# Kernel optimization log

Hardware: AMD Instinct MI355X
Metric: run time of the kernel (lower is better)

## Reference

```python
import jax, jax.numpy as jnp
import numpy as np
import math

# Model hyperparameters (SchNet defaults)
H = 128        # hidden_channels
F = 128        # num_filters
G = 50         # num_gaussians
CUT = 6.0      # cutoff (Angstrom)
L_INT = 3      # num_interactions
# Graph scale
N_MOL = 512    # molecules
APM = 32       # atoms per molecule
N = N_MOL * APM
BOX = 10.0     # side of cubic box per molecule


def _ssp(x):
    # ShiftedSoftplus
    return jax.nn.softplus(x) - math.log(2.0)


def setup_inputs() -> dict:
    rng = np.random.default_rng(0)
    pos = rng.uniform(0.0, BOX, (N_MOL, APM, 3)).astype(np.float32)
    # radius graph within each molecule (faithful to radius_graph_custom,
    # precomputed here because edge count is data-dependent)
    srcs, dsts = [], []
    for m in range(N_MOL):
        p = pos[m]
        dm = np.linalg.norm(p[:, None, :] - p[None, :, :], axis=-1)
        mask = dm <= CUT
        np.fill_diagonal(mask, False)
        s, t = np.nonzero(mask)
        srcs.append(s + m * APM)
        dsts.append(t + m * APM)
    edge_index = np.stack([np.concatenate(srcs), np.concatenate(dsts)]).astype(np.int32)
    pos = pos.reshape(N, 3)
    batch = np.repeat(np.arange(N_MOL, dtype=np.int32), APM)
    z = rng.integers(1, 100, N).astype(np.int32)

    key = jax.random.key(0)
    ks = jax.random.split(key, 16)
    s = 0.1
    nrm = lambda k, shp: (jax.random.normal(k, shp, dtype=jnp.float32) * s)
    return {
        "z": jnp.asarray(z),
        "pos": jnp.asarray(pos),
        "batch": jnp.asarray(batch),
        "edge_index": jnp.asarray(edge_index),
        "emb": nrm(ks[0], (100, H)),
        "mlp_w1": nrm(ks[1], (L_INT, G, F)),
        "mlp_b1": jnp.zeros((L_INT, F), jnp.float32),
        "mlp_w2": nrm(ks[2], (L_INT, F, F)),
        "mlp_b2": jnp.zeros((L_INT, F), jnp.float32),
        "cf1_w": nrm(ks[3], (L_INT, H, F)),
        "cf2_w": nrm(ks[4], (L_INT, F, H)),
        "cf2_b": jnp.zeros((L_INT, H), jnp.float32),
        "lin_w": nrm(ks[5], (L_INT, H, H)),
        "lin_b": jnp.zeros((L_INT, H), jnp.float32),
        "out1_w": nrm(ks[6], (H, H // 2)),
        "out1_b": jnp.zeros((H // 2,), jnp.float32),
        "out2_w": nrm(ks[7], (H // 2, 1)),
        "out2_b": jnp.zeros((1,), jnp.float32),
    }


def reference(z, pos, batch, edge_index, emb,
              mlp_w1, mlp_b1, mlp_w2, mlp_b2,
              cf1_w, cf2_w, cf2_b, lin_w, lin_b,
              out1_w, out1_b, out2_w, out2_b):
    src, dst = edge_index[0], edge_index[1]
    # edge_weight = euclidean distance (== cdist[src, dst])
    d = jnp.sqrt(jnp.sum((pos[src] - pos[dst]) ** 2, axis=-1))  # [E]
    # GaussianSmearing
    offs = jnp.linspace(0.0, CUT, G)
    coeff = -0.5 / (CUT / (G - 1)) ** 2
    edge_attr = jnp.exp(coeff * (d[:, None] - offs[None, :]) ** 2)  # [E, G]
    # cosine cutoff
    Ccut = 0.5 * (jnp.cos(d * math.pi / CUT) + 1.0)  # [E]

    h = emb[z]  # [N, H]
    for l in range(L_INT):
        # edge filter MLP with cutoff
        W = _ssp(edge_attr @ mlp_w1[l] + mlp_b1[l]) @ mlp_w2[l] + mlp_b2[l]  # [E, F]
        W = W * Ccut[:, None]
        # CFConv: lin1 -> gather x_j -> multiply -> scatter-add to dst -> lin2
        msg = (h @ cf1_w[l])[src] * W                                # [E, F]
        agg = jax.ops.segment_sum(msg, dst, num_segments=N)          # [N, F]
        v = agg @ cf2_w[l] + cf2_b[l]                                # [N, H]
        v = _ssp(v)
        v = v @ lin_w[l] + lin_b[l]
        h = h + v  # residual

    h = _ssp(h @ out1_w + out1_b)
    h = h @ out2_w + out2_b                                          # [N, 1]
    out = jax.ops.segment_sum(h, batch, num_segments=N_MOL)          # [N_MOL, 1]
    return out
```

## Files before the change

kernel.cpp:

```cpp
#include <hip/hip_runtime.h>
#include <hip/hip_bf16.h>
#include <math.h>

#define NATOMS 16384
#define NMOL   512
#define APM    32
#define GDIM   50
#define KTAB   4096
#define MAXEPM 1000

#define STRH 132
#define STRA 136

typedef __attribute__((ext_vector_type(8))) short   short8;
typedef __attribute__((ext_vector_type(4))) float   floatx4;

__device__ __forceinline__ float ssp(float x) {
    float e = __expf(-fabsf(x));
    return fmaxf(x, 0.0f) + __logf(1.0f + e) - 0.69314718055994531f;
}

__device__ __forceinline__ unsigned short f2bf(float x) {
    union { float f; unsigned int u; } v; v.f = x;
    unsigned int lsb = (v.u >> 16) & 1u;
    v.u += 0x7fffu + lsb;
    return (unsigned short)(v.u >> 16);
}

__device__ __forceinline__ unsigned int pk2bf(float a, float b) {
    __hip_bfloat162 h = __float22bfloat162_rn(make_float2(a, b));
    unsigned int u;
    __builtin_memcpy(&u, &h, 4);
    return u;
}

#define KW1 72
#define KW2 136
#define NTILE (KTAB / 64)

__global__ __launch_bounds__(256) void mega_setup_kernel(
    const float* __restrict__ pos, const int* __restrict__ eidx, int E, int EB,
    int* __restrict__ rowptr,
    const float* __restrict__ cf1, const float* __restrict__ cf2,
    const float* __restrict__ lin, const float* __restrict__ out1,
    unsigned short* __restrict__ Wtall, unsigned int* __restrict__ meta,
    const float* __restrict__ w1_, const float* __restrict__ b1_,
    const float* __restrict__ w2_, const float* __restrict__ b2_,
    unsigned short* __restrict__ Tt)
{
    const int WB = (9 * 16384 + 64 * 128 + 255) / 256;
    const int b = blockIdx.x;
    const int tid = threadIdx.x;

    if (b < EB) {
        int idx = b * 256 + tid;
        if (idx < E) {
            int s = eidx[idx], t = eidx[E + idx];
            float dx = pos[3 * s]     - pos[3 * t];
            float dy = pos[3 * s + 1] - pos[3 * t + 1];
            float dz = pos[3 * s + 2] - pos[3 * t + 2];
            float d  = sqrtf(dx * dx + dy * dy + dz * dz);
            float u  = d * (float)(KTAB - 1) / 6.0f;
            int i = min((int)(u + 0.5f), KTAB - 1);
            meta[idx] = ((unsigned)i << 6) | (unsigned)(t & 31);
        } else if (idx < E + NATOMS + 1) {
            int a = idx - E;
            int lo = 0, hi = E;
            while (lo < hi) { int mid = (lo + hi) >> 1; if (eidx[mid] < a) lo = mid + 1; else hi = mid; }
            rowptr[a] = lo;
        }
        return;
    }
    if (b < EB + WB) {
        int idx = (b - EB) * 256 + tid;
        if (idx < 9 * 16384) {
            int wi = idx >> 14, rem = idx & 16383;
            int n = rem >> 7, k = rem & 127;
            int l = wi / 3, which = wi % 3;
            const float* src = (which == 0) ? cf1 : (which == 1) ? cf2 : lin;
            Wtall[idx] = f2bf(src[(size_t)l * 16384 + k * 128 + n]);
        } else if (idx < 9 * 16384 + 64 * 128) {
            int q = idx - 9 * 16384;
            int n = q >> 7, k = q & 127;
            Wtall[idx] = f2bf(out1[k * 64 + n]);
        }
        return;
    }

    __shared__ unsigned short s_bufA[128 * KW2];
    __shared__ unsigned short s_bufB[128 * KW1];

    const int tt = b - EB - WB;
    const int l  = tt / NTILE;
    const int bx = tt % NTILE;
    const float* w1 = w1_ + (size_t)l * GDIM * 128;
    const float* b1 = b1_ + (size_t)l * 128;
    const float* w2 = w2_ + (size_t)l * 128 * 128;
    const float* b2 = b2_ + (size_t)l * 128;
    unsigned short* Tg = Tt + (size_t)l * KTAB * 128;

    unsigned short* s_w1T = s_bufB;
    unsigned short* s_w2T = s_bufA;
    unsigned short* s_t   = s_bufB;

    for (int i = tid; i < GDIM * 128; i += 256) {
        int g = i >> 7, f = i & 127;
        s_w1T[f * KW1 + g] = f2bf(w1[i]);
    }
    for (int i = tid; i < (64 - GDIM) * 128; i += 256) {
        int g = GDIM + (i >> 7), f = i & 127;
        s_w1T[f * KW1 + g] = 0;
    }
    for (int i = tid; i < 128 * 128; i += 256) {
        int k = i >> 7, n = i & 127;
        s_w2T[n * KW2 + k] = f2bf(w2[i]);
    }

    const int lane = tid & 63;
    const int w    = tid >> 6;
    const int l15  = lane & 15;
    const int quad = lane >> 4;

    float b1v[8], b2v[8];
    #pragma unroll
    for (int nt = 0; nt < 8; nt++) {
        b1v[nt] = b1[nt * 16 + l15];
        b2v[nt] = b2[nt * 16 + l15];
    }
    __syncthreads();

    const float hstep = 6.0f / (float)(KTAB - 1);
    const float step  = 6.0f / 49.0f;
    const float coeff = -0.5f / (step * step);
    const float pioc  = 3.14159265358979323846f / 6.0f;
    const int k0 = bx * 64;
    const float dm = (float)(k0 + w * 16 + l15) * hstep;

    floatx4 acc1[8];
    #pragma unroll
    for (int nt = 0; nt < 8; nt++) acc1[nt] = (floatx4){0.f, 0.f, 0.f, 0.f};
    #pragma unroll
    for (int ks = 0; ks < 2; ks++) {
        unsigned int ap[4];
        #pragma unroll
        for (int jj = 0; jj < 4; jj++) {
            int g0 = ks * 32 + quad * 8 + 2 * jj;
            float d0 = dm - (float)g0 * step;
            float d1 = dm - (float)(g0 + 1) * step;
            float v0 = (g0 < GDIM)     ? __expf(coeff * d0 * d0) : 0.0f;
            float v1 = (g0 + 1 < GDIM) ? __expf(coeff * d1 * d1) : 0.0f;
            ap[jj] = pk2bf(v0, v1);
        }
        short8 af;
        __builtin_memcpy(&af, ap, 16);
        #pragma unroll
        for (int nt = 0; nt < 8; nt++) {
            short8 bfg = *(const short8*)&s_w1T[(nt * 16 + l15) * KW1 + ks * 32 + quad * 8];
            acc1[nt] = __builtin_amdgcn_mfma_f32_16x16x32_bf16(af, bfg, acc1[nt], 0, 0, 0);
        }
    }
    __syncthreads();

    #pragma unroll
    for (int nt = 0; nt < 8; nt++) {
        #pragma unroll
        for (int r = 0; r < 4; r++) {
            int row = w * 16 + quad * 4 + r;
            s_t[row * KW2 + nt * 16 + l15] = f2bf(ssp(acc1[nt][r] + b1v[nt]));
        }
    }

    floatx4 acc2[8];
    #pragma unroll
    for (int nt = 0; nt < 8; nt++) acc2[nt] = (floatx4){0.f, 0.f, 0.f, 0.f};
    #pragma unroll
    for (int ks = 0; ks < 4; ks++) {
        short8 af = *(const short8*)&s_t[(w * 16 + l15) * KW2 + ks * 32 + quad * 8];
        #pragma unroll
        for (int nt = 0; nt < 8; nt++) {
            short8 bfg = *(const short8*)&s_w2T[(nt * 16 + l15) * KW2 + ks * 32 + quad * 8];
            acc2[nt] = __builtin_amdgcn_mfma_f32_16x16x32_bf16(af, bfg, acc2[nt], 0, 0, 0);
        }
    }

    #pragma unroll
    for (int nt = 0; nt < 8; nt++) {
        #pragma unroll
        for (int r = 0; r < 4; r++) {
            int row = w * 16 + quad * 4 + r;
            float d = (float)(k0 + row) * hstep;
            float cut = 0.5f * (__cosf(d * pioc) + 1.0f);
            Tg[(size_t)(k0 + row) * 128 + nt * 16 + l15] = f2bf((acc2[nt][r] + b2v[nt]) * cut);
        }
    }
}

__global__ __launch_bounds__(512, 4) void fused_schnet_kernel(
    const int* __restrict__ z, const float* __restrict__ emb,
    const int* __restrict__ rowptr, const unsigned int* __restrict__ meta,
    const unsigned short* __restrict__ Tt,
    const unsigned short* __restrict__ Wtall,
    const float* __restrict__ cf2_b, const float* __restrict__ lin_b,
    const float* __restrict__ out1_b, const float* __restrict__ out2_w,
    const float* __restrict__ out2_b,
    float* __restrict__ out)
{
    __shared__ float s_h[32 * STRH];
    __shared__ float s_hx[33 * 128];
    __shared__ unsigned short s_agg[32 * STRA];
    __shared__ unsigned int s_meta[MAXEPM];
    __shared__ float s_red;
    unsigned short* s_t = (unsigned short*)s_hx;

    const int tid  = threadIdx.x;
    const int lane = tid & 63;
    const int w    = tid >> 6;
    const int l15  = lane & 15;
    const int quad = lane >> 4;
    const int r16  = (w & 1) * 16;
    const int c32  = (w >> 1) * 32;
    const int B0   = blockIdx.x * 32;

    for (int i = tid; i < 32 * 128; i += 512) {
        int row = i >> 7, col = i & 127;
        s_h[row * STRH + col] = emb[(size_t)z[B0 + row] * 128 + col];
    }
    if (tid < 128) s_hx[32 * 128 + tid] = 0.0f;
    if (tid == 0) s_red = 0.0f;

    const int ebase = rowptr[B0];
    const int nE    = rowptr[B0 + 32] - ebase;
    for (int i = tid; i < nE; i += 512) s_meta[i] = meta[ebase + i];
    if (tid == 0) s_meta[nE] = 32u;

    const int rp = rowptr[B0 + w * 4 + min(lane, 4)] - ebase;

    const unsigned short* WtO = Wtall + 9 * 16384;

    for (int l = 0; l < 3; l++) {
        const unsigned short* W1 = Wtall + (size_t)(l * 3 + 0) * 16384;
        const unsigned short* W2 = Wtall + (size_t)(l * 3 + 1) * 16384;
        const unsigned short* W3 = Wtall + (size_t)(l * 3 + 2) * 16384;
        const unsigned short* Ttl = Tt + (size_t)l * KTAB * 128;

        __syncthreads();

        floatx4 acc[2];
        #pragma unroll
        for (int nt = 0; nt < 2; nt++) acc[nt] = (floatx4){0.f, 0.f, 0.f, 0.f};
        #pragma unroll
        for (int ks = 0; ks < 4; ks++) {
            const float* hp = &s_h[(r16 + l15) * STRH + ks * 32 + quad * 8];
            float4 xa = *(const float4*)hp;
            float4 xb = *(const float4*)(hp + 4);
            unsigned int ap[4];
            ap[0] = pk2bf(xa.x, xa.y); ap[1] = pk2bf(xa.z, xa.w);
            ap[2] = pk2bf(xb.x, xb.y); ap[3] = pk2bf(xb.z, xb.w);
            short8 af;
            __builtin_memcpy(&af, ap, 16);
            #pragma unroll
            for (int nt = 0; nt < 2; nt++) {
                short8 bfg = *(const short8*)&W1[(size_t)(c32 + nt * 16 + l15) * 128 + ks * 32 + quad * 8];
                acc[nt] = __builtin_amdgcn_mfma_f32_16x16x32_bf16(af, bfg, acc[nt], 0, 0, 0);
            }
        }
        #pragma unroll
        for (int nt = 0; nt < 2; nt++) {
            #pragma unroll
            for (int r = 0; r < 4; r++)
                s_hx[(r16 + quad * 4 + r) * 128 + c32 + nt * 16 + l15] = acc[nt][r];
        }

        __syncthreads();

        for (int al = 0; al < 4; al++) {
            const int e0 = __shfl(rp, al);
            const int e1 = __shfl(rp, al + 1);
            float ax[8], ay[8];
            #pragma unroll
            for (int j = 0; j < 8; j++) { ax[j] = 0.f; ay[j] = 0.f; }
            for (int e = e0; e < e1; e += 8) {
                #pragma unroll
                for (int j = 0; j < 8; j++) {
                    int idx = (e + j < e1) ? (e + j) : nE;
                    unsigned int q = s_meta[idx];
                    int tl   = q & 63;
                    int knot = q >> 6;
                    unsigned int tp = *(const unsigned int*)&Ttl[((size_t)knot << 7) + 2 * lane];
                    float2 hv = *(const float2*)&s_hx[(tl << 7) + 2 * lane];
                    ax[j] = fmaf(hv.x, __uint_as_float(tp << 16), ax[j]);
                    ay[j] = fmaf(hv.y, __uint_as_float(tp & 0xffff0000u), ay[j]);
                }
            }
            float sx = ((ax[0] + ax[1]) + (ax[2] + ax[3])) + ((ax[4] + ax[5]) + (ax[6] + ax[7]));
            float sy = ((ay[0] + ay[1]) + (ay[2] + ay[3])) + ((ay[4] + ay[5]) + (ay[6] + ay[7]));
            *(unsigned int*)&s_agg[(w * 4 + al) * STRA + 2 * lane] = pk2bf(sx, sy);
        }

        __syncthreads();

        float bva[2], bvb[2];
        #pragma unroll
        for (int nt = 0; nt < 2; nt++) {
            bva[nt] = cf2_b[l * 128 + c32 + nt * 16 + l15];
            bvb[nt] = lin_b[l * 128 + c32 + nt * 16 + l15];
        }
        #pragma unroll
        for (int nt = 0; nt < 2; nt++) acc[nt] = (floatx4){0.f, 0.f, 0.f, 0.f};
        #pragma unroll
        for (int ks = 0; ks < 4; ks++) {
            short8 af = *(const short8*)&s_agg[(r16 + l15) * STRA + ks * 32 + quad * 8];
            #pragma unroll
            for (int nt = 0; nt < 2; nt++) {
                short8 bfg = *(const short8*)&W2[(size_t)(c32 + nt * 16 + l15) * 128 + ks * 32 + quad * 8];
                acc[nt] = __builtin_amdgcn_mfma_f32_16x16x32_bf16(af, bfg, acc[nt], 0, 0, 0);
            }
        }
        #pragma unroll
        for (int nt = 0; nt < 2; nt++) {
            #pragma unroll
            for (int r = 0; r < 4; r++) {
                int row = r16 + quad * 4 + r;
                s_t[row * STRA + c32 + nt * 16 + l15] = f2bf(ssp(acc[nt][r] + bva[nt]));
            }
        }

        __syncthreads();

        #pragma unroll
        for (int nt = 0; nt < 2; nt++) acc[nt] = (floatx4){0.f, 0.f, 0.f, 0.f};
        #pragma unroll
        for (int ks = 0; ks < 4; ks++) {
            short8 af = *(const short8*)&s_t[(r16 + l15) * STRA + ks * 32 + quad * 8];
            #pragma unroll
            for (int nt = 0; nt < 2; nt++) {
                short8 bfg = *(const short8*)&W3[(size_t)(c32 + nt * 16 + l15) * 128 + ks * 32 + quad * 8];
                acc[nt] = __builtin_amdgcn_mfma_f32_16x16x32_bf16(af, bfg, acc[nt], 0, 0, 0);
            }
        }
        #pragma unroll
        for (int nt = 0; nt < 2; nt++) {
            #pragma unroll
            for (int r = 0; r < 4; r++) {
                int row = r16 + quad * 4 + r;
                s_h[row * STRH + c32 + nt * 16 + l15] += acc[nt][r] + bvb[nt];
            }
        }
    }

    __syncthreads();

    const int c16 = (w >> 1) * 16;
    floatx4 ha = (floatx4){0.f, 0.f, 0.f, 0.f};
    #pragma unroll
    for (int ks = 0; ks < 4; ks++) {
        const float* hp = &s_h[(r16 + l15) * STRH + ks * 32 + quad * 8];
        float4 xa = *(const float4*)hp;
        float4 xb = *(const float4*)(hp + 4);
        unsigned int ap[4];
        ap[0] = pk2bf(xa.x, xa.y); ap[1] = pk2bf(xa.z, xa.w);
        ap[2] = pk2bf(xb.x, xb.y); ap[3] = pk2bf(xb.z, xb.w);
        short8 af;
        __builtin_memcpy(&af, ap, 16);
        short8 bfg = *(const short8*)&WtO[(size_t)(c16 + l15) * 128 + ks * 32 + quad * 8];
        ha = __builtin_amdgcn_mfma_f32_16x16x32_bf16(af, bfg, ha, 0, 0, 0);
    }
    float part = 0.0f;
    {
        float b1o = out1_b[c16 + l15];
        float o2  = out2_w[c16 + l15];
        #pragma unroll
        for (int r = 0; r < 4; r++)
            part += ssp(ha[r] + b1o) * o2;
    }
    #pragma unroll
    for (int off = 32; off > 0; off >>= 1) part += __shfl_down(part, off);
    if (lane == 0) atomicAdd(&s_red, part);
    __syncthreads();
    if (tid == 0) out[blockIdx.x] = s_red + 32.0f * out2_b[0];
}

extern "C" void kernel_launch(void* const* d_in, const int* in_sizes, int n_in,
                              void* d_out, int out_size, void* d_ws, size_t ws_size,
                              hipStream_t stream)
{
    const int*   z      = (const int*)d_in[0];
    const float* pos    = (const float*)d_in[1];
    const int*   eidx   = (const int*)d_in[3];
    const float* emb    = (const float*)d_in[4];
    const float* mlp_w1 = (const float*)d_in[5];
    const float* mlp_b1 = (const float*)d_in[6];
    const float* mlp_w2 = (const float*)d_in[7];
    const float* mlp_b2 = (const float*)d_in[8];
    const float* cf1_w  = (const float*)d_in[9];
    const float* cf2_w  = (const float*)d_in[10];
    const float* cf2_b  = (const float*)d_in[11];
    const float* lin_w  = (const float*)d_in[12];
    const float* lin_b  = (const float*)d_in[13];
    const float* out1_w = (const float*)d_in[14];
    const float* out1_b = (const float*)d_in[15];
    const float* out2_w = (const float*)d_in[16];
    const float* out2_b = (const float*)d_in[17];
    const int E = in_sizes[3] / 2;

    char* p = (char*)d_ws;
    unsigned int* meta = (unsigned int*)p;        p += ((size_t)(E + 1) * 4 + 63) & ~63ULL;
    unsigned short* Tt = (unsigned short*)p;      p += (size_t)3 * KTAB * 128 * 2;
    int* rowptr = (int*)p;                        p += ((size_t)(NATOMS + 1) * 4 + 63) & ~63ULL;
    unsigned short* Wtall = (unsigned short*)p;

    const int EB = (E + NATOMS + 1 + 255) / 256;
    const int WB = (9 * 16384 + 64 * 128 + 255) / 256;
    const int TB = NTILE * 3;
    mega_setup_kernel<<<EB + WB + TB, 256, 0, stream>>>(
        pos, eidx, E, EB, rowptr, cf1_w, cf2_w, lin_w, out1_w, Wtall, meta,
        mlp_w1, mlp_b1, mlp_w2, mlp_b2, Tt);

    fused_schnet_kernel<<<NMOL, 512, 0, stream>>>(
        z, emb, rowptr, meta, Tt, Wtall,
        cf2_b, lin_b, out1_b, out2_w, out2_b, (float*)d_out);
}
```

Before: 171.0 us.

## Use per-atom padded edge slots and split edges across wave halves

The edge metadata is packed with the source atom so each edge can be placed into a fixed 32-slot region per destination atom in shared memory. Slots are prefilled with byte offsets that point at a zero row. In the aggregation loop, each half-wave handles alternate edges and each lane reads 4 feature channels (uint2 table, float4 hidden) instead of 2. The two halves are combined with a cross-half shuffle, which removes per-edge bounds selects and halves the loop trip count. The cost is an extra sync, the cross-half shuffle, and an assumption that no atom has more than 32 edges.

```diff
diff --git a/kernel.cpp b/kernel.cpp
--- a/kernel.cpp
+++ b/kernel.cpp
@@ -7,7 +7,6 @@
 #define APM    32
 #define GDIM   50
 #define KTAB   4096
-#define MAXEPM 1000
 
 #define STRH 132
 #define STRA 136
@@ -62,7 +61,7 @@
             float d  = sqrtf(dx * dx + dy * dy + dz * dz);
             float u  = d * (float)(KTAB - 1) / 6.0f;
             int i = min((int)(u + 0.5f), KTAB - 1);
-            meta[idx] = ((unsigned)i << 6) | (unsigned)(t & 31);
+            meta[idx] = ((unsigned)i << 10) | ((unsigned)(s & 31) << 5) | (unsigned)(t & 31);
         } else if (idx < E + NATOMS + 1) {
             int a = idx - E;
             int lo = 0, hi = E;
@@ -208,7 +207,7 @@
     __shared__ float s_h[32 * STRH];
     __shared__ float s_hx[33 * 128];
     __shared__ unsigned short s_agg[32 * STRA];
-    __shared__ unsigned int s_meta[MAXEPM];
+    __shared__ uint2 s_meta2[32 * 32];
     __shared__ float s_red;
     unsigned short* s_t = (unsigned short*)s_hx;
 
@@ -221,27 +220,42 @@
     const int c32  = (w >> 1) * 32;
     const int B0   = blockIdx.x * 32;
 
+    const int half = lane >> 5;
+    const int l31  = lane & 31;
+    const unsigned tOff = (unsigned)(l31 << 3);
+    const unsigned hOff = (unsigned)(l31 << 4);
+
     for (int i = tid; i < 32 * 128; i += 512) {
         int row = i >> 7, col = i & 127;
         s_h[row * STRH + col] = emb[(size_t)z[B0 + row] * 128 + col];
     }
     if (tid < 128) s_hx[32 * 128 + tid] = 0.0f;
     if (tid == 0) s_red = 0.0f;
+    for (int i = tid; i < 32 * 32; i += 512)
+        s_meta2[i] = make_uint2(0u, 32u << 9);
 
     const int ebase = rowptr[B0];
     const int nE    = rowptr[B0 + 32] - ebase;
-    for (int i = tid; i < nE; i += 512) s_meta[i] = meta[ebase + i];
-    if (tid == 0) s_meta[nE] = 32u;
+
+    __syncthreads();
+
+    for (int i = tid; i < nE; i += 512) {
+        unsigned q = meta[ebase + i];
+        int a = (int)((q >> 5) & 31u);
+        int slot = i - (rowptr[B0 + a] - ebase);
+        s_meta2[(a << 5) + slot] = make_uint2((q >> 10) << 8, (q & 31u) << 9);
+    }
 
     const int rp = rowptr[B0 + w * 4 + min(lane, 4)] - ebase;
 
     const unsigned short* WtO = Wtall + 9 * 16384;
+    const char* hxB = (const char*)s_hx;
 
     for (int l = 0; l < 3; l++) {
         const unsigned short* W1 = Wtall + (size_t)(l * 3 + 0) * 16384;
         const unsigned short* W2 = Wtall + (size_t)(l * 3 + 1) * 16384;
         const unsigned short* W3 = Wtall + (size_t)(l * 3 + 2) * 16384;
-        const unsigned short* Ttl = Tt + (size_t)l * KTAB * 128;
+        const char* TlB = (const char*)(Tt + (size_t)l * KTAB * 128);
 
         __syncthreads();
 
@@ -274,27 +288,40 @@
         __syncthreads();
 
         for (int al = 0; al < 4; al++) {
-            const int e0 = __shfl(rp, al);
-            const int e1 = __shfl(rp, al + 1);
-            float ax[8], ay[8];
-            #pragma unroll
-            for (int j = 0; j < 8; j++) { ax[j] = 0.f; ay[j] = 0.f; }
-            for (int e = e0; e < e1; e += 8) {
+            const int atom = w * 4 + al;
+            const int deg  = __shfl(rp, al + 1) - __shfl(rp, al);
+            const uint2* mp = &s_meta2[(atom << 5) + half];
+            float pa[4][4];
+            #pragma unroll
+            for (int j = 0; j < 4; j++) {
                 #pragma unroll
-                for (int j = 0; j < 8; j++) {
-                    int idx = (e + j < e1) ? (e + j) : nE;
-                    unsigned int q = s_meta[idx];
-                    int tl   = q & 63;
-                    int knot = q >> 6;
-                    unsigned int tp = *(const unsigned int*)&Ttl[((size_t)knot << 7) + 2 * lane];
-                    float2 hv = *(const float2*)&s_hx[(tl << 7) + 2 * lane];
-                    ax[j] = fmaf(hv.x, __uint_as_float(tp << 16), ax[j]);
-                    ay[j] = fmaf(hv.y, __uint_as_float(tp & 0xffff0000u), ay[j]);
+                for (int c = 0; c < 4; c++) pa[j][c] = 0.0f;
+            }
+            const int nb = (deg + 7) >> 3;
+            for (int bb = 0; bb < nb; bb++) {
+                #pragma unroll
+                for (int j = 0; j < 4; j++) {
+                    uint2 m  = mp[(bb << 3) + (j << 1)];
+                    uint2 tp = *(const uint2*)(TlB + (m.x + tOff));
+                    float4 hv = *(const float4*)(hxB + (m.y + hOff));
+                    pa[j][0] = fmaf(hv.x, __uint_as_float(tp.x << 16),         pa[j][0]);
+                    pa[j][1] = fmaf(hv.y, __uint_as_float(tp.x & 0xffff0000u), pa[j][1]);
+                    pa[j][2] = fmaf(hv.z, __uint_as_float(tp.y << 16),         pa[j][2]);
+                    pa[j][3] = fmaf(hv.w, __uint_as_float(tp.y & 0xffff0000u), pa[j][3]);
                 }
             }
-            float sx = ((ax[0] + ax[1]) + (ax[2] + ax[3])) + ((ax[4] + ax[5]) + (ax[6] + ax[7]));
-            float sy = ((ay[0] + ay[1]) + (ay[2] + ay[3])) + ((ay[4] + ay[5]) + (ay[6] + ay[7]));
-            *(unsigned int*)&s_agg[(w * 4 + al) * STRA + 2 * lane] = pk2bf(sx, sy);
+            float c0 = (pa[0][0] + pa[1][0]) + (pa[2][0] + pa[3][0]);
+            float c1 = (pa[0][1] + pa[1][1]) + (pa[2][1] + pa[3][1]);
+            float c2 = (pa[0][2] + pa[1][2]) + (pa[2][2] + pa[3][2]);
+            float c3 = (pa[0][3] + pa[1][3]) + (pa[2][3] + pa[3][3]);
+            c0 += __shfl_xor(c0, 32);
+            c1 += __shfl_xor(c1, 32);
+            c2 += __shfl_xor(c2, 32);
+            c3 += __shfl_xor(c3, 32);
+            if (half == 0) {
+                uint2 pk = make_uint2(pk2bf(c0, c1), pk2bf(c2, c3));
+                *(uint2*)&s_agg[atom * STRA + (l31 << 2)] = pk;
+            }
         }
 
         __syncthreads();
```

Measured after the change: 178.2 us. 4.2% more time.
